# Performance work log

Measured on AMD Instinct MI355X. Metric: run time of the kernel, lower is better.

Reference implementation:

```python
import jax, jax.numpy as jnp
import numpy as np

N, E = 100000, 400000
IN_DIM, PAD_DIM, HID = 384, 3, 64

def _xavier(key, fan_in, fan_out, shape=None):
    shape = shape or (fan_in, fan_out)
    lim = float(np.sqrt(6.0 / (fan_in + fan_out)))
    return jax.random.uniform(key, shape, jnp.float32, -lim, lim)

def setup_inputs():
    key = jax.random.key(0)
    ks = jax.random.split(key, 20)
    return {
        "x": jax.random.normal(ks[0], (N, IN_DIM), jnp.float32),
        "edge_index": jax.random.randint(ks[1], (2, E), 0, N),
        "pad_state": jax.random.uniform(ks[2], (PAD_DIM,), jnp.float32, -1.0, 1.0),
        # GAT layer 1: in = IN_DIM+PAD_DIM, heads=4, out=HID per head
        "W1": _xavier(ks[3], IN_DIM + PAD_DIM, 4 * HID),
        "att_src1": _xavier(ks[4], HID, HID, (4, HID)),
        "att_dst1": _xavier(ks[5], HID, HID, (4, HID)),
        "b1": jnp.zeros((4 * HID,), jnp.float32),
        # GAT layer 2: in = 4*HID, heads=2
        "W2": _xavier(ks[6], 4 * HID, 2 * HID),
        "att_src2": _xavier(ks[7], HID, HID, (2, HID)),
        "att_dst2": _xavier(ks[8], HID, HID, (2, HID)),
        "b2": jnp.zeros((2 * HID,), jnp.float32),
        # attention-score MLP
        "aw1": _xavier(ks[9], 2 * HID, HID),
        "ab1": jnp.zeros((HID,), jnp.float32),
        "aw2": _xavier(ks[10], HID, 1),
        "ab2": jnp.zeros((1,), jnp.float32),
        # emotion gate
        "gw": _xavier(ks[11], PAD_DIM, HID),
        "gb": jnp.zeros((HID,), jnp.float32),
    }

def _gat(h_in, src, dst, W, a_src, a_dst, bias, heads):
    # PyG GATConv (eval mode): linear -> per-head LeakyReLU attention logits
    # -> edge softmax over destination -> scatter-add aggregation -> concat heads + bias
    n = h_in.shape[0]
    h = (h_in @ W).reshape(n, heads, -1)               # [N,H,C]
    al_s = jnp.einsum('nhc,hc->nh', h, a_src)          # [N,H]
    al_d = jnp.einsum('nhc,hc->nh', h, a_dst)
    e = jax.nn.leaky_relu(al_s[src] + al_d[dst], 0.2)  # [Etot,H]
    m = jax.ops.segment_max(e, dst, num_segments=n)    # stable softmax per dst
    p = jnp.exp(e - m[dst])
    denom = jax.ops.segment_sum(p, dst, num_segments=n)
    coef = p / (denom[dst] + 1e-16)
    out = jax.ops.segment_sum(h[src] * coef[:, :, None], dst, num_segments=n)
    return out.reshape(n, -1) + bias

def reference(x, edge_index, pad_state, W1, att_src1, att_dst1, b1,
              W2, att_src2, att_dst2, b2, aw1, ab1, aw2, ab2, gw, gb):
    n = x.shape[0]
    loops = jnp.arange(n, dtype=edge_index.dtype)      # add_self_loops=True default
    src = jnp.concatenate([edge_index[0], loops])
    dst = jnp.concatenate([edge_index[1], loops])
    pad_exp = jnp.broadcast_to(pad_state.reshape(1, -1), (n, pad_state.size))
    h = jnp.concatenate([x, pad_exp], axis=-1)         # [N, in_dim+pad_dim]
    h = jax.nn.elu(_gat(h, src, dst, W1, att_src1, att_dst1, b1, 4))
    h = jax.nn.elu(_gat(h, src, dst, W2, att_src2, att_dst2, b2, 2))
    gate = jax.nn.sigmoid(pad_exp @ gw + gb)           # [N,HID]
    h = h * jnp.tile(gate, (1, 2))                     # [N,2*HID]
    attn = jax.nn.sigmoid(jax.nn.relu(h @ aw1 + ab1) @ aw2 + ab2)  # [N,1]
    return h, attn
```

## Files before the change

### kernel.cpp

```cpp
#include <hip/hip_runtime.h>
#include <hip/hip_bf16.h>
#include <stdint.h>

#define IN_DIM 384
#define HID 64
#define C1 256
#define C2 128

typedef unsigned int uint32;
typedef __bf16 bf16x8 __attribute__((ext_vector_type(8)));
typedef float f32x4 __attribute__((ext_vector_type(4)));

static __device__ __forceinline__ float bf2f(unsigned short u){
    return __uint_as_float(((uint32)u) << 16);
}
static __device__ __forceinline__ unsigned short f2bf(float x){
    uint32 u = __float_as_uint(x);
    return (unsigned short)((u + 0x7FFFu + ((u >> 16) & 1u)) >> 16);
}
static __device__ __forceinline__ uint32 pack2(float a, float b){
    return (uint32)f2bf(a) | ((uint32)f2bf(b) << 16);
}

__global__ void k_zero(int* deg, int* cur, int N){
    int i = blockIdx.x*256 + threadIdx.x;
    if (i < N){ deg[i] = 0; cur[i] = 0; }
}
__global__ void k_hist(const int* __restrict__ ei, int* deg, int E){
    int i = blockIdx.x*256 + threadIdx.x;
    if (i < E) atomicAdd(&deg[ei[E + i]], 1);
}
__global__ void k_scan1(const int* __restrict__ deg, int* rowptr, int* part, int N){
    __shared__ int s[256];
    int tid = threadIdx.x;
    int i = blockIdx.x*256 + tid;
    int v = (i < N) ? deg[i] : 0;
    s[tid] = v; __syncthreads();
    for (int off = 1; off < 256; off <<= 1){
        int t = (tid >= off) ? s[tid - off] : 0;
        __syncthreads();
        s[tid] += t;
        __syncthreads();
    }
    if (i < N) rowptr[i] = s[tid] - v;
    if (tid == 255) part[blockIdx.x] = s[tid];
}
__global__ void k_scan2(int* part, int nb){
    __shared__ int s[512];
    int tid = threadIdx.x;
    int v = (tid < nb) ? part[tid] : 0;
    s[tid] = v; __syncthreads();
    for (int off = 1; off < 512; off <<= 1){
        int t = (tid >= off) ? s[tid - off] : 0;
        __syncthreads();
        s[tid] += t;
        __syncthreads();
    }
    if (tid < nb) part[tid] = s[tid] - v;
}
__global__ void k_scan3(int* rowptr, const int* __restrict__ part, int N, int E){
    int i = blockIdx.x*256 + threadIdx.x;
    if (i < N) rowptr[i] += part[blockIdx.x];
    if (i == 0) rowptr[N] = E;
}
__global__ void k_scatter(const int* __restrict__ ei, const int* __restrict__ rowptr,
                          int* cur, int* colx, int* dstx, int E){
    int i = blockIdx.x*256 + threadIdx.x;
    if (i < E){
        int d = ei[E + i];
        int pos = atomicAdd(&cur[d], 1);
        int p = rowptr[d] + pos;
        colx[p] = ei[i];
        dstx[p] = d;
    }
}

__global__ __launch_bounds__(256) void k_cvtW(const float* __restrict__ W,
        unsigned short* __restrict__ Wf, int ncol, int ntiles, int nunits){
    int unit = blockIdx.x*4 + (threadIdx.x >> 6);
    if (unit >= nunits) return;
    int l = threadIdx.x & 63;
    int s = unit / ntiles, ct = unit % ntiles;
    int col = ct*16 + (l & 15);
    int g = l >> 4;
    unsigned short o[8];
    #pragma unroll
    for (int j = 0; j < 8; j++){
        int k = s*32 + g*8 + j;
        o[j] = f2bf(W[(size_t)k*ncol + col]);
    }
    ushort4* dst = (ushort4*)&Wf[((size_t)unit*64 + l)*8];
    dst[0] = make_ushort4(o[0], o[1], o[2], o[3]);
    dst[1] = make_ushort4(o[4], o[5], o[6], o[7]);
}

__global__ __launch_bounds__(256) void k_prep(const float* __restrict__ W1,
        const float* __restrict__ pad, const float* __restrict__ gw, const float* __restrict__ gb,
        float* __restrict__ c1v, float* __restrict__ gate){
    int tid = threadIdx.x;
    c1v[tid] = pad[0]*W1[(size_t)(IN_DIM+0)*C1 + tid]
             + pad[1]*W1[(size_t)(IN_DIM+1)*C1 + tid]
             + pad[2]*W1[(size_t)(IN_DIM+2)*C1 + tid];
    if (tid < HID){
        float g = pad[0]*gw[0*HID + tid] + pad[1]*gw[1*HID + tid] + pad[2]*gw[2*HID + tid] + gb[tid];
        gate[tid] = 1.f/(1.f + __expf(-g));
    }
}

__global__ __launch_bounds__(256) void k_gemm1_mfma(const float* __restrict__ x,
        const unsigned short* __restrict__ Wf, const float* __restrict__ c1v,
        const float* __restrict__ as1, const float* __restrict__ ad1,
        unsigned short* __restrict__ h1, float* __restrict__ als, float* __restrict__ ald, int N)
{
    __shared__ unsigned short Af[2][4*64*8];
    const int tid = threadIdx.x;
    const int l   = tid & 63;
    const int w   = tid >> 6;
    const int n0  = blockIdx.x * 64;

    const int sr  = tid >> 2;
    const int kc  = tid & 3;
    const int d0  = ((sr >> 4)*64 + kc*16 + (sr & 15))*8;
    int crow = n0 + sr; if (crow > N-1) crow = N-1;
    const float* xrow = x + (size_t)crow*IN_DIM + kc*8;

    f32x4 acc[4][4];
    #pragma unroll
    for (int i = 0; i < 4; i++)
        #pragma unroll
        for (int rt = 0; rt < 4; rt++)
            acc[i][rt] = (f32x4){0.f, 0.f, 0.f, 0.f};

    float4 ra, rb;
    uint4 wcur[4], wnxt[4];

    ra = *(const float4*)(xrow + 0); rb = *(const float4*)(xrow + 4);
    {
        uint4 u;
        u.x = pack2(ra.x, ra.y); u.y = pack2(ra.z, ra.w);
        u.z = pack2(rb.x, rb.y); u.w = pack2(rb.z, rb.w);
        *(uint4*)&Af[0][d0] = u;
    }
    {
        const unsigned short* p = Wf + ((size_t)(w*4)*64 + l)*8;
        #pragma unroll
        for (int i = 0; i < 4; i++) wcur[i] = *(const uint4*)(p + (size_t)i*512);
    }
    __syncthreads();

    for (int s = 0; s < 12; ++s){
        if (s < 11){
            const float* src = xrow + (s+1)*32;
            ra = *(const float4*)(src + 0); rb = *(const float4*)(src + 4);
            const unsigned short* p = Wf + ((size_t)((s+1)*16 + w*4)*64 + l)*8;
            #pragma unroll
            for (int i = 0; i < 4; i++) wnxt[i] = *(const uint4*)(p + (size_t)i*512);
        }
        bf16x8 af[4];
        #pragma unroll
        for (int rt = 0; rt < 4; rt++)
            af[rt] = __builtin_bit_cast(bf16x8, *(const uint4*)&Af[s&1][(rt*64 + l)*8]);
        #pragma unroll
        for (int i = 0; i < 4; i++){
            bf16x8 bw = __builtin_bit_cast(bf16x8, wcur[i]);
            #pragma unroll
            for (int rt = 0; rt < 4; rt++)
                acc[i][rt] = __builtin_amdgcn_mfma_f32_16x16x32_bf16(bw, af[rt], acc[i][rt], 0, 0, 0);
        }
        if (s < 11){
            uint4 u;
            u.x = pack2(ra.x, ra.y); u.y = pack2(ra.z, ra.w);
            u.z = pack2(rb.x, rb.y); u.w = pack2(rb.z, rb.w);
            *(uint4*)&Af[(s+1)&1][d0] = u;
            __syncthreads();
            #pragma unroll
            for (int i = 0; i < 4; i++) wcur[i] = wnxt[i];
        }
    }

    const int g = l >> 4;
    float4 cvv[4], av[4], dv[4];
    #pragma unroll
    for (int i = 0; i < 4; i++){
        int cl = i*16 + g*4;
        cvv[i] = *(const float4*)&c1v[w*64 + cl];
        av[i]  = *(const float4*)&as1[w*64 + cl];
        dv[i]  = *(const float4*)&ad1[w*64 + cl];
    }
    #pragma unroll
    for (int rt = 0; rt < 4; rt++){
        int node = n0 + rt*16 + (l & 15);
        bool ok = node < N;
        float ps = 0.f, pd = 0.f;
        #pragma unroll
        for (int i = 0; i < 4; i++){
            float h0 = acc[i][rt][0] + cvv[i].x;
            float h1v = acc[i][rt][1] + cvv[i].y;
            float h2v = acc[i][rt][2] + cvv[i].z;
            float h3v = acc[i][rt][3] + cvv[i].w;
            ps += h0*av[i].x + h1v*av[i].y + h2v*av[i].z + h3v*av[i].w;
            pd += h0*dv[i].x + h1v*dv[i].y + h2v*dv[i].z + h3v*dv[i].w;
            if (ok){
                ushort4 o = make_ushort4(f2bf(h0), f2bf(h1v), f2bf(h2v), f2bf(h3v));
                *(ushort4*)&h1[(size_t)node*C1 + w*64 + i*16 + g*4] = o;
            }
        }
        ps += __shfl_xor(ps, 16, 64); ps += __shfl_xor(ps, 32, 64);
        pd += __shfl_xor(pd, 16, 64); pd += __shfl_xor(pd, 32, 64);
        if (ok && g == 0){
            als[(size_t)node*4 + w] = ps;
            ald[(size_t)node*4 + w] = pd;
        }
    }
}

__global__ __launch_bounds__(256) void k_gemm2_mfma(const unsigned short* __restrict__ x2,
        const unsigned short* __restrict__ Wf,
        const float* __restrict__ as2, const float* __restrict__ ad2,
        unsigned short* __restrict__ h2, float* __restrict__ als, float* __restrict__ ald, int N)
{
    __shared__ unsigned short Af[2][4*64*8];
    const int tid = threadIdx.x;
    const int l   = tid & 63;
    const int w   = tid >> 6;
    const int wr  = w >> 1, wc = w & 1;
    const int n0  = blockIdx.x * 64;

    const int sr  = tid >> 2;
    const int kc  = tid & 3;
    const int d0  = ((sr >> 4)*64 + kc*16 + (sr & 15))*8;
    int crow = n0 + sr; if (crow > N-1) crow = N-1;
    const unsigned short* xrow = x2 + (size_t)crow*C1 + kc*8;

    f32x4 acc[4][2];
    #pragma unroll
    for (int i = 0; i < 4; i++)
        #pragma unroll
        for (int rt = 0; rt < 2; rt++)
            acc[i][rt] = (f32x4){0.f, 0.f, 0.f, 0.f};

    uint4 p0, wcur[4], wnxt[4];
    p0 = *(const uint4*)(xrow);
    *(uint4*)&Af[0][d0] = p0;
    {
        const unsigned short* p = Wf + ((size_t)(wc*4)*64 + l)*8;
        #pragma unroll
        for (int i = 0; i < 4; i++) wcur[i] = *(const uint4*)(p + (size_t)i*512);
    }
    __syncthreads();

    for (int s = 0; s < 8; ++s){
        if (s < 7){
            p0 = *(const uint4*)(xrow + (s+1)*32);
            const unsigned short* p = Wf + ((size_t)((s+1)*8 + wc*4)*64 + l)*8;
            #pragma unroll
            for (int i = 0; i < 4; i++) wnxt[i] = *(const uint4*)(p + (size_t)i*512);
        }
        bf16x8 af[2];
        #pragma unroll
        for (int rt = 0; rt < 2; rt++)
            af[rt] = __builtin_bit_cast(bf16x8, *(const uint4*)&Af[s&1][((wr*2 + rt)*64 + l)*8]);
        #pragma unroll
        for (int i = 0; i < 4; i++){
            bf16x8 bw = __builtin_bit_cast(bf16x8, wcur[i]);
            #pragma unroll
            for (int rt = 0; rt < 2; rt++)
                acc[i][rt] = __builtin_amdgcn_mfma_f32_16x16x32_bf16(bw, af[rt], acc[i][rt], 0, 0, 0);
        }
        if (s < 7){
            *(uint4*)&Af[(s+1)&1][d0] = p0;
            __syncthreads();
            #pragma unroll
            for (int i = 0; i < 4; i++) wcur[i] = wnxt[i];
        }
    }

    const int g = l >> 4;
    float4 av[4], dv[4];
    #pragma unroll
    for (int i = 0; i < 4; i++){
        int cl = i*16 + g*4;
        av[i] = *(const float4*)&as2[wc*64 + cl];
        dv[i] = *(const float4*)&ad2[wc*64 + cl];
    }
    #pragma unroll
    for (int rt = 0; rt < 2; rt++){
        int node = n0 + wr*32 + rt*16 + (l & 15);
        bool ok = node < N;
        float ps = 0.f, pd = 0.f;
        #pragma unroll
        for (int i = 0; i < 4; i++){
            float h0 = acc[i][rt][0], h1v = acc[i][rt][1];
            float h2v = acc[i][rt][2], h3v = acc[i][rt][3];
            ps += h0*av[i].x + h1v*av[i].y + h2v*av[i].z + h3v*av[i].w;
            pd += h0*dv[i].x + h1v*dv[i].y + h2v*dv[i].z + h3v*dv[i].w;
            if (ok){
                ushort4 o = make_ushort4(f2bf(h0), f2bf(h1v), f2bf(h2v), f2bf(h3v));
                *(ushort4*)&h2[(size_t)node*C2 + wc*64 + i*16 + g*4] = o;
            }
        }
        ps += __shfl_xor(ps, 16, 64); ps += __shfl_xor(ps, 32, 64);
        pd += __shfl_xor(pd, 16, 64); pd += __shfl_xor(pd, 32, 64);
        if (ok && g == 0){
            als[(size_t)node*2 + wc] = ps;
            ald[(size_t)node*2 + wc] = pd;
        }
    }
}

template<int H>
__global__ __launch_bounds__(256) void k_elogit(const int* __restrict__ colx,
        const int* __restrict__ dstx, const float* __restrict__ als,
        const float* __restrict__ ald, float* __restrict__ ep, int E)
{
    int i = blockIdx.x*256 + threadIdx.x;
    if (i >= E) return;
    int s = colx[i], d = dstx[i];
    if constexpr (H == 4){
        float4 a = *(const float4*)&als[(size_t)s*4];
        float4 b = *(const float4*)&ald[(size_t)d*4];
        float4 e;
        e.x = a.x + b.x; e.x = fmaxf(e.x, 0.2f*e.x);
        e.y = a.y + b.y; e.y = fmaxf(e.y, 0.2f*e.y);
        e.z = a.z + b.z; e.z = fmaxf(e.z, 0.2f*e.z);
        e.w = a.w + b.w; e.w = fmaxf(e.w, 0.2f*e.w);
        *(float4*)&ep[(size_t)i*4] = e;
    } else {
        float2 a = *(const float2*)&als[(size_t)s*2];
        float2 b = *(const float2*)&ald[(size_t)d*2];
        float2 e;
        e.x = a.x + b.x; e.x = fmaxf(e.x, 0.2f*e.x);
        e.y = a.y + b.y; e.y = fmaxf(e.y, 0.2f*e.y);
        *(float2*)&ep[(size_t)i*2] = e;
    }
}

template<int H>
__global__ __launch_bounds__(256) void k_segsm(const int* __restrict__ rowptr,
        const float* __restrict__ als, const float* __restrict__ ald,
        float* __restrict__ ep, float* __restrict__ den, float* __restrict__ pSelf, int NH)
{
    int t = blockIdx.x*256 + threadIdx.x;
    if (t >= NH) return;
    int node = t / H;
    int head = t - node*H;
    int base = rowptr[node];
    int cnt  = rowptr[node+1] - base;
    float es = als[t] + ald[t];
    es = fmaxf(es, 0.2f*es);
    float m = es;
    for (int j = 0; j < cnt; j++)
        m = fmaxf(m, ep[(size_t)(base + j)*H + head]);
    float ps = __expf(es - m);
    float dn = ps;
    for (int j = 0; j < cnt; j++){
        size_t idx = (size_t)(base + j)*H + head;
        float p = __expf(ep[idx] - m);
        ep[idx] = p;
        dn += p;
    }
    den[t]   = dn;
    pSelf[t] = ps;
}

template<int H, int CPL, int LAYER>
__global__ __launch_bounds__(256) void k_gat(const unsigned short* __restrict__ hlin,
        const float* __restrict__ ep, const float* __restrict__ den, const float* __restrict__ pSelf,
        const int* __restrict__ rowptr, const int* __restrict__ colx,
        const float* __restrict__ bias, const float* __restrict__ gate,
        unsigned short* __restrict__ out_bf, float* __restrict__ out_f, int N)
{
    constexpr int C = H*64;
    constexpr uint32 RB = C*2;
    int lane = threadIdx.x & 63, wid = threadIdx.x >> 6;
    int n = blockIdx.x*4 + wid;
    if (n >= N) return;
    const int c0 = lane*CPL;
    const int head = c0 >> 6;
    const int base = rowptr[n];
    const int cnt  = rowptr[n+1] - base;
    const char* hbase = (const char*)hlin + (uint32)c0*2;

    float acc[CPL];
    {
        float psf = pSelf[(uint32)n*H + head];
        if constexpr (CPL == 4){
            ushort4 v = *(const ushort4*)(hbase + (size_t)(uint32)n*RB);
            acc[0] = psf*bf2f(v.x); acc[1] = psf*bf2f(v.y);
            acc[2] = psf*bf2f(v.z); acc[3] = psf*bf2f(v.w);
        } else {
            uint32 v = *(const uint32*)(hbase + (size_t)(uint32)n*RB);
            acc[0] = psf*bf2f((unsigned short)(v & 0xffff));
            acc[1] = psf*bf2f((unsigned short)(v >> 16));
        }
    }
    for (int i = 0; i < cnt; i += 4){
        int idx[4], sk[4];
        #pragma unroll
        for (int k = 0; k < 4; k++){
            int ii = i + k; if (ii > cnt-1) ii = cnt-1;
            idx[k] = base + ii;
        }
        #pragma unroll
        for (int k = 0; k < 4; k++) sk[k] = colx[idx[k]];
        float pk[4];
        #pragma unroll
        for (int k = 0; k < 4; k++){
            float pv = ep[(size_t)(uint32)idx[k]*H + head];
            pk[k] = (i + k < cnt) ? pv : 0.f;
        }
        if constexpr (CPL == 4){
            ushort4 h4[4];
            #pragma unroll
            for (int k = 0; k < 4; k++) h4[k] = *(const ushort4*)(hbase + (size_t)(uint32)sk[k]*RB);
            #pragma unroll
            for (int k = 0; k < 4; k++){
                acc[0] += pk[k]*bf2f(h4[k].x);
                acc[1] += pk[k]*bf2f(h4[k].y);
                acc[2] += pk[k]*bf2f(h4[k].z);
                acc[3] += pk[k]*bf2f(h4[k].w);
            }
        } else {
            uint32 h2v[4];
            #pragma unroll
            for (int k = 0; k < 4; k++) h2v[k] = *(const uint32*)(hbase + (size_t)(uint32)sk[k]*RB);
            #pragma unroll
            for (int k = 0; k < 4; k++){
                acc[0] += pk[k]*bf2f((unsigned short)(h2v[k] & 0xffff));
                acc[1] += pk[k]*bf2f((unsigned short)(h2v[k] >> 16));
            }
        }
    }

    float inv = 1.f/(den[(uint32)n*H + head] + 1e-16f);
    if constexpr (LAYER == 1){
        unsigned short o[CPL];
        #pragma unroll
        for (int j = 0; j < CPL; j++){
            float r = acc[j]*inv + bias[c0 + j];
            r = (r > 0.f) ? r : (__expf(r) - 1.f);
            o[j] = f2bf(r);
        }
        if constexpr (CPL == 4){
            ushort4 ov; ov.x = o[0]; ov.y = o[1]; ov.z = o[2]; ov.w = o[3];
            *(ushort4*)&out_bf[(size_t)n*C + c0] = ov;
        }
    } else {
        float o[CPL];
        #pragma unroll
        for (int j = 0; j < CPL; j++){
            float r = acc[j]*inv + bias[c0 + j];
            r = (r > 0.f) ? r : (__expf(r) - 1.f);
            o[j] = r*gate[(c0 + j) & 63];
        }
        if constexpr (CPL == 2){
            *(float2*)&out_f[(size_t)n*C + c0] = make_float2(o[0], o[1]);
        }
    }
}

__global__ __launch_bounds__(256) void k_attn_mfma(const float* __restrict__ outh,
        const unsigned short* __restrict__ Wfa, const float* __restrict__ ab1,
        const float* __restrict__ aw2, const float* __restrict__ ab2,
        float* __restrict__ attn, int N)
{
    __shared__ unsigned short Af[4*8*64*8];
    const int tid = threadIdx.x;
    const int l   = tid & 63;
    const int w   = tid >> 6;
    const int n0  = blockIdx.x * 128;

    const int r  = tid >> 1;
    const int kh = tid & 1;
    const int rt8 = r >> 4, rr = r & 15;
    int crow = n0 + r; if (crow > N-1) crow = N-1;
    const float* src = outh + (size_t)crow*C2 + kh*16;
    #pragma unroll
    for (int s = 0; s < 4; s++){
        float4 a = *(const float4*)(src + s*32 + 0);
        float4 b = *(const float4*)(src + s*32 + 4);
        float4 c = *(const float4*)(src + s*32 + 8);
        float4 d = *(const float4*)(src + s*32 + 12);
        uint4 u0, u1;
        u0.x = pack2(a.x, a.y); u0.y = pack2(a.z, a.w);
        u0.z = pack2(b.x, b.y); u0.w = pack2(b.z, b.w);
        u1.x = pack2(c.x, c.y); u1.y = pack2(c.z, c.w);
        u1.z = pack2(d.x, d.y); u1.w = pack2(d.z, d.w);
        int d0 = ((s*8 + rt8)*64 + (kh*2)*16 + rr)*8;
        *(uint4*)&Af[d0]       = u0;
        *(uint4*)&Af[d0 + 128] = u1;
    }
    __syncthreads();

    f32x4 acc[4][2];
    #pragma unroll
    for (int i = 0; i < 4; i++)
        #pragma unroll
        for (int rt = 0; rt < 2; rt++)
            acc[i][rt] = (f32x4){0.f, 0.f, 0.f, 0.f};

    #pragma unroll
    for (int s = 0; s < 4; s++){
        bf16x8 af[2];
        #pragma unroll
        for (int rt = 0; rt < 2; rt++)
            af[rt] = __builtin_bit_cast(bf16x8, *(const uint4*)&Af[((s*8 + w*2 + rt)*64 + l)*8]);
        #pragma unroll
        for (int i = 0; i < 4; i++){
            bf16x8 bw = __builtin_bit_cast(bf16x8, *(const uint4*)&Wfa[((size_t)(s*4 + i)*64 + l)*8]);
            #pragma unroll
            for (int rt = 0; rt < 2; rt++)
                acc[i][rt] = __builtin_amdgcn_mfma_f32_16x16x32_bf16(bw, af[rt], acc[i][rt], 0, 0, 0);
        }
    }

    const int g = l >> 4;
    float4 abv[4], awv[4];
    #pragma unroll
    for (int i = 0; i < 4; i++){
        abv[i] = *(const float4*)&ab1[i*16 + g*4];
        awv[i] = *(const float4*)&aw2[i*16 + g*4];
    }
    float b2v = ab2[0];
    #pragma unroll
    for (int rt = 0; rt < 2; rt++){
        int node = n0 + (w*2 + rt)*16 + (l & 15);
        float part = 0.f;
        #pragma unroll
        for (int i = 0; i < 4; i++){
            float v0 = fmaxf(acc[i][rt][0] + abv[i].x, 0.f);
            float v1 = fmaxf(acc[i][rt][1] + abv[i].y, 0.f);
            float v2 = fmaxf(acc[i][rt][2] + abv[i].z, 0.f);
            float v3 = fmaxf(acc[i][rt][3] + abv[i].w, 0.f);
            part += v0*awv[i].x + v1*awv[i].y + v2*awv[i].z + v3*awv[i].w;
        }
        part += __shfl_xor(part, 16, 64);
        part += __shfl_xor(part, 32, 64);
        if (g == 0 && node < N)
            attn[node] = 1.f/(1.f + __expf(-(part + b2v)));
    }
}

extern "C" void kernel_launch(void* const* d_in, const int* in_sizes, int n_in,
                              void* d_out, int out_size, void* d_ws, size_t ws_size,
                              hipStream_t stream)
{
    const float* x    = (const float*)d_in[0];
    const int*   ei   = (const int*)  d_in[1];
    const float* pad  = (const float*)d_in[2];
    const float* W1   = (const float*)d_in[3];
    const float* as1  = (const float*)d_in[4];
    const float* ad1  = (const float*)d_in[5];
    const float* b1   = (const float*)d_in[6];
    const float* W2   = (const float*)d_in[7];
    const float* as2  = (const float*)d_in[8];
    const float* ad2  = (const float*)d_in[9];
    const float* b2   = (const float*)d_in[10];
    const float* aw1  = (const float*)d_in[11];
    const float* ab1  = (const float*)d_in[12];
    const float* aw2  = (const float*)d_in[13];
    const float* ab2  = (const float*)d_in[14];
    const float* gw   = (const float*)d_in[15];
    const float* gb   = (const float*)d_in[16];

    const int N = in_sizes[0] / IN_DIM;
    const int E = in_sizes[1] / 2;

    float* outh    = (float*)d_out;
    float* outattn = outh + (size_t)N*C2;

    char* w = (char*)d_ws;
    auto alloc = [&](size_t bytes)->char*{
        char* p = w;
        w += (bytes + 255) & ~(size_t)255;
        return p;
    };
    unsigned short* h1  = (unsigned short*)alloc((size_t)N*C1*2);
    unsigned short* x2  = (unsigned short*)alloc((size_t)N*C1*2);
    unsigned short* h2  = (unsigned short*)alloc((size_t)N*C2*2);
    float* als1 = (float*)alloc((size_t)N*4*4);
    float* ald1 = (float*)alloc((size_t)N*4*4);
    float* als2 = (float*)alloc((size_t)N*2*4);
    float* ald2 = (float*)alloc((size_t)N*2*4);
    int* deg    = (int*)alloc((size_t)N*4);
    int* cur    = (int*)alloc((size_t)N*4);
    int* rowptr = (int*)alloc((size_t)(N+1)*4);
    int* colx   = (int*)alloc((size_t)E*4);
    int* dstx   = (int*)alloc((size_t)E*4);
    int* part   = (int*)alloc(512*4);
    unsigned short* Wf1 = (unsigned short*)alloc((size_t)12*16*64*8*2);
    unsigned short* Wf2 = (unsigned short*)alloc((size_t)8*8*64*8*2);
    unsigned short* Wfa = (unsigned short*)alloc((size_t)4*4*64*8*2);
    float* c1v  = (float*)alloc(C1*4);
    float* gate = (float*)alloc(HID*4);

    float* ep1    = (float*)h2;
    float* den1   = (float*)((char*)h2 + (size_t)E*16);
    float* pSelf1 = (float*)((char*)h2 + (size_t)E*16 + (size_t)N*16);
    float* ep2    = (float*)x2;
    float* den2   = (float*)((char*)x2 + (size_t)E*8);
    float* pSelf2 = (float*)((char*)x2 + (size_t)E*8 + (size_t)N*8);

    const int nbN = (N + 255)/256;
    const int nbE = (E + 255)/256;
    const int nbW = (N + 3)/4;
    const int nbG = (N + 63)/64;
    const int nbA = (N + 127)/128;

    k_cvtW <<<(192+3)/4, 256, 0, stream>>>(W1, Wf1, C1, 16, 192);
    k_cvtW <<<(64+3)/4,  256, 0, stream>>>(W2, Wf2, C2, 8, 64);
    k_cvtW <<<(16+3)/4,  256, 0, stream>>>(aw1, Wfa, HID, 4, 16);
    k_prep <<<1, 256, 0, stream>>>(W1, pad, gw, gb, c1v, gate);

    k_zero   <<<nbN, 256, 0, stream>>>(deg, cur, N);
    k_hist   <<<nbE, 256, 0, stream>>>(ei, deg, E);
    k_scan1  <<<nbN, 256, 0, stream>>>(deg, rowptr, part, N);
    k_scan2  <<<1, 512, 0, stream>>>(part, nbN);
    k_scan3  <<<nbN, 256, 0, stream>>>(rowptr, part, N, E);
    k_scatter<<<nbE, 256, 0, stream>>>(ei, rowptr, cur, colx, dstx, E);

    k_gemm1_mfma<<<nbG, 256, 0, stream>>>(x, Wf1, c1v, as1, ad1, h1, als1, ald1, N);
    k_elogit<4><<<nbE, 256, 0, stream>>>(colx, dstx, als1, ald1, ep1, E);
    k_segsm<4> <<<(N*4 + 255)/256, 256, 0, stream>>>(rowptr, als1, ald1, ep1, den1, pSelf1, N*4);
    k_gat<4,4,1><<<nbW, 256, 0, stream>>>(h1, ep1, den1, pSelf1, rowptr, colx, b1,
                                          nullptr, x2, nullptr, N);

    k_gemm2_mfma<<<nbG, 256, 0, stream>>>(x2, Wf2, as2, ad2, h2, als2, ald2, N);
    k_elogit<2><<<nbE, 256, 0, stream>>>(colx, dstx, als2, ald2, ep2, E);
    k_segsm<2> <<<(N*2 + 255)/256, 256, 0, stream>>>(rowptr, als2, ald2, ep2, den2, pSelf2, N*2);
    k_gat<2,2,2><<<nbW, 256, 0, stream>>>(h2, ep2, den2, pSelf2, rowptr, colx, b2,
                                          gate, nullptr, outh, N);

    k_attn_mfma<<<nbA, 256, 0, stream>>>(outh, Wfa, ab1, aw2, ab2, outattn, N);
}
```

Baseline: 288.6 us.

## Restructure GEMM kernels so each wave owns 16 rows and all output columns

Both GEMM kernels drop the shared-memory double-buffered A tile and the per-step block barriers. Each wave now loads its own 16 node rows directly from global memory into registers and computes every output column, reading all weight fragments from global/L2 memory. This removes LDS traffic and __syncthreads, and lets the attention-logit partials for all heads be written as one vector store per node. In exchange, weight-fragment loads per wave grow four-fold (layer 1) and the accumulator register count rises, which may lower occupancy.

Result: slower. 579.2 us (+100.7%).

```diff
diff --git a/kernel.cpp b/kernel.cpp
--- a/kernel.cpp
+++ b/kernel.cpp
@@ -112,105 +112,68 @@
         const float* __restrict__ as1, const float* __restrict__ ad1,
         unsigned short* __restrict__ h1, float* __restrict__ als, float* __restrict__ ald, int N)
 {
-    __shared__ unsigned short Af[2][4*64*8];
     const int tid = threadIdx.x;
     const int l   = tid & 63;
     const int w   = tid >> 6;
     const int n0  = blockIdx.x * 64;
 
-    const int sr  = tid >> 2;
-    const int kc  = tid & 3;
-    const int d0  = ((sr >> 4)*64 + kc*16 + (sr & 15))*8;
-    int crow = n0 + sr; if (crow > N-1) crow = N-1;
-    const float* xrow = x + (size_t)crow*IN_DIM + kc*8;
-
-    f32x4 acc[4][4];
-    #pragma unroll
-    for (int i = 0; i < 4; i++)
-        #pragma unroll
-        for (int rt = 0; rt < 4; rt++)
-            acc[i][rt] = (f32x4){0.f, 0.f, 0.f, 0.f};
-
-    float4 ra, rb;
-    uint4 wcur[4], wnxt[4];
-
-    ra = *(const float4*)(xrow + 0); rb = *(const float4*)(xrow + 4);
-    {
-        uint4 u;
-        u.x = pack2(ra.x, ra.y); u.y = pack2(ra.z, ra.w);
-        u.z = pack2(rb.x, rb.y); u.w = pack2(rb.z, rb.w);
-        *(uint4*)&Af[0][d0] = u;
-    }
-    {
-        const unsigned short* p = Wf + ((size_t)(w*4)*64 + l)*8;
-        #pragma unroll
-        for (int i = 0; i < 4; i++) wcur[i] = *(const uint4*)(p + (size_t)i*512);
-    }
-    __syncthreads();
-
-    for (int s = 0; s < 12; ++s){
-        if (s < 11){
-            const float* src = xrow + (s+1)*32;
-            ra = *(const float4*)(src + 0); rb = *(const float4*)(src + 4);
-            const unsigned short* p = Wf + ((size_t)((s+1)*16 + w*4)*64 + l)*8;
-            #pragma unroll
-            for (int i = 0; i < 4; i++) wnxt[i] = *(const uint4*)(p + (size_t)i*512);
-        }
-        bf16x8 af[4];
-        #pragma unroll
-        for (int rt = 0; rt < 4; rt++)
-            af[rt] = __builtin_bit_cast(bf16x8, *(const uint4*)&Af[s&1][(rt*64 + l)*8]);
-        #pragma unroll
-        for (int i = 0; i < 4; i++){
-            bf16x8 bw = __builtin_bit_cast(bf16x8, wcur[i]);
-            #pragma unroll
-            for (int rt = 0; rt < 4; rt++)
-                acc[i][rt] = __builtin_amdgcn_mfma_f32_16x16x32_bf16(bw, af[rt], acc[i][rt], 0, 0, 0);
-        }
-        if (s < 11){
-            uint4 u;
-            u.x = pack2(ra.x, ra.y); u.y = pack2(ra.z, ra.w);
-            u.z = pack2(rb.x, rb.y); u.w = pack2(rb.z, rb.w);
-            *(uint4*)&Af[(s+1)&1][d0] = u;
-            __syncthreads();
-            #pragma unroll
-            for (int i = 0; i < 4; i++) wcur[i] = wnxt[i];
+    const int node = n0 + w*16 + (l & 15);
+    int crow = node; if (crow > N-1) crow = N-1;
+    const float* xr = x + (size_t)crow*IN_DIM + (l >> 4)*8;
+
+    f32x4 acc[16];
+    #pragma unroll
+    for (int i = 0; i < 16; i++) acc[i] = (f32x4){0.f, 0.f, 0.f, 0.f};
+
+    float4 a0 = *(const float4*)(xr);
+    float4 a1 = *(const float4*)(xr + 4);
+
+    for (int ku = 0; ku < 12; ++ku){
+        uint4 af;
+        af.x = pack2(a0.x, a0.y); af.y = pack2(a0.z, a0.w);
+        af.z = pack2(a1.x, a1.y); af.w = pack2(a1.z, a1.w);
+        if (ku < 11){
+            a0 = *(const float4*)(xr + (ku+1)*32);
+            a1 = *(const float4*)(xr + (ku+1)*32 + 4);
+        }
+        bf16x8 afb = __builtin_bit_cast(bf16x8, af);
+        const unsigned short* wp = Wf + ((size_t)(ku*16)*64 + l)*8;
+        #pragma unroll
+        for (int i = 0; i < 16; i++){
+            bf16x8 bw = __builtin_bit_cast(bf16x8, *(const uint4*)(wp + (size_t)i*512));
+            acc[i] = __builtin_amdgcn_mfma_f32_16x16x32_bf16(bw, afb, acc[i], 0, 0, 0);
         }
     }
 
     const int g = l >> 4;
-    float4 cvv[4], av[4], dv[4];
-    #pragma unroll
-    for (int i = 0; i < 4; i++){
-        int cl = i*16 + g*4;
-        cvv[i] = *(const float4*)&c1v[w*64 + cl];
-        av[i]  = *(const float4*)&as1[w*64 + cl];
-        dv[i]  = *(const float4*)&ad1[w*64 + cl];
-    }
-    #pragma unroll
-    for (int rt = 0; rt < 4; rt++){
-        int node = n0 + rt*16 + (l & 15);
-        bool ok = node < N;
-        float ps = 0.f, pd = 0.f;
-        #pragma unroll
-        for (int i = 0; i < 4; i++){
-            float h0 = acc[i][rt][0] + cvv[i].x;
-            float h1v = acc[i][rt][1] + cvv[i].y;
-            float h2v = acc[i][rt][2] + cvv[i].z;
-            float h3v = acc[i][rt][3] + cvv[i].w;
-            ps += h0*av[i].x + h1v*av[i].y + h2v*av[i].z + h3v*av[i].w;
-            pd += h0*dv[i].x + h1v*dv[i].y + h2v*dv[i].z + h3v*dv[i].w;
-            if (ok){
-                ushort4 o = make_ushort4(f2bf(h0), f2bf(h1v), f2bf(h2v), f2bf(h3v));
-                *(ushort4*)&h1[(size_t)node*C1 + w*64 + i*16 + g*4] = o;
-            }
-        }
-        ps += __shfl_xor(ps, 16, 64); ps += __shfl_xor(ps, 32, 64);
-        pd += __shfl_xor(pd, 16, 64); pd += __shfl_xor(pd, 32, 64);
-        if (ok && g == 0){
-            als[(size_t)node*4 + w] = ps;
-            ald[(size_t)node*4 + w] = pd;
-        }
+    const bool ok = node < N;
+    float ps[4] = {0.f,0.f,0.f,0.f}, pd[4] = {0.f,0.f,0.f,0.f};
+    #pragma unroll
+    for (int i = 0; i < 16; i++){
+        int col = i*16 + g*4;
+        float4 cv = *(const float4*)&c1v[col];
+        float4 av = *(const float4*)&as1[col];
+        float4 dv = *(const float4*)&ad1[col];
+        float h0 = acc[i][0] + cv.x;
+        float h1v = acc[i][1] + cv.y;
+        float h2v = acc[i][2] + cv.z;
+        float h3v = acc[i][3] + cv.w;
+        int h = i >> 2;
+        ps[h] += h0*av.x + h1v*av.y + h2v*av.z + h3v*av.w;
+        pd[h] += h0*dv.x + h1v*dv.y + h2v*dv.z + h3v*dv.w;
+        if (ok){
+            ushort4 o = make_ushort4(f2bf(h0), f2bf(h1v), f2bf(h2v), f2bf(h3v));
+            *(ushort4*)&h1[(size_t)node*C1 + col] = o;
+        }
+    }
+    #pragma unroll
+    for (int h = 0; h < 4; h++){
+        ps[h] += __shfl_xor(ps[h], 16, 64); ps[h] += __shfl_xor(ps[h], 32, 64);
+        pd[h] += __shfl_xor(pd[h], 16, 64); pd[h] += __shfl_xor(pd[h], 32, 64);
+    }
+    if (ok && g == 0){
+        *(float4*)&als[(size_t)node*4] = make_float4(ps[0], ps[1], ps[2], ps[3]);
+        *(float4*)&ald[(size_t)node*4] = make_float4(pd[0], pd[1], pd[2], pd[3]);
     }
 }
 
@@ -219,92 +182,57 @@
         const float* __restrict__ as2, const float* __restrict__ ad2,
         unsigned short* __restrict__ h2, float* __restrict__ als, float* __restrict__ ald, int N)
 {
-    __shared__ unsigned short Af[2][4*64*8];
     const int tid = threadIdx.x;
     const int l   = tid & 63;
     const int w   = tid >> 6;
-    const int wr  = w >> 1, wc = w & 1;
     const int n0  = blockIdx.x * 64;
 
-    const int sr  = tid >> 2;
-    const int kc  = tid & 3;
-    const int d0  = ((sr >> 4)*64 + kc*16 + (sr & 15))*8;
-    int crow = n0 + sr; if (crow > N-1) crow = N-1;
-    const unsigned short* xrow = x2 + (size_t)crow*C1 + kc*8;
-
-    f32x4 acc[4][2];
-    #pragma unroll
-    for (int i = 0; i < 4; i++)
-        #pragma unroll
-        for (int rt = 0; rt < 2; rt++)
-            acc[i][rt] = (f32x4){0.f, 0.f, 0.f, 0.f};
-
-    uint4 p0, wcur[4], wnxt[4];
-    p0 = *(const uint4*)(xrow);
-    *(uint4*)&Af[0][d0] = p0;
-    {
-        const unsigned short* p = Wf + ((size_t)(wc*4)*64 + l)*8;
-        #pragma unroll
-        for (int i = 0; i < 4; i++) wcur[i] = *(const uint4*)(p + (size_t)i*512);
-    }
-    __syncthreads();
-
-    for (int s = 0; s < 8; ++s){
-        if (s < 7){
-            p0 = *(const uint4*)(xrow + (s+1)*32);
-            const unsigned short* p = Wf + ((size_t)((s+1)*8 + wc*4)*64 + l)*8;
-            #pragma unroll
-            for (int i = 0; i < 4; i++) wnxt[i] = *(const uint4*)(p + (size_t)i*512);
-        }
-        bf16x8 af[2];
-        #pragma unroll
-        for (int rt = 0; rt < 2; rt++)
-            af[rt] = __builtin_bit_cast(bf16x8, *(const uint4*)&Af[s&1][((wr*2 + rt)*64 + l)*8]);
-        #pragma unroll
-        for (int i = 0; i < 4; i++){
-            bf16x8 bw = __builtin_bit_cast(bf16x8, wcur[i]);
-            #pragma unroll
-            for (int rt = 0; rt < 2; rt++)
-                acc[i][rt] = __builtin_amdgcn_mfma_f32_16x16x32_bf16(bw, af[rt], acc[i][rt], 0, 0, 0);
-        }
-        if (s < 7){
-            *(uint4*)&Af[(s+1)&1][d0] = p0;
-            __syncthreads();
-            #pragma unroll
-            for (int i = 0; i < 4; i++) wcur[i] = wnxt[i];
+    const int node = n0 + w*16 + (l & 15);
+    int crow = node; if (crow > N-1) crow = N-1;
+    const unsigned short* xr = x2 + (size_t)crow*C1 + (l >> 4)*8;
+
+    f32x4 acc[8];
+    #pragma unroll
+    for (int i = 0; i < 8; i++) acc[i] = (f32x4){0.f, 0.f, 0.f, 0.f};
+
+    uint4 a0 = *(const uint4*)(xr);
+
+    for (int ku = 0; ku < 8; ++ku){
+        bf16x8 afb = __builtin_bit_cast(bf16x8, a0);
+        if (ku < 7) a0 = *(const uint4*)(xr + (ku+1)*32);
+        const unsigned short* wp = Wf + ((size_t)(ku*8)*64 + l)*8;
+        #pragma unroll
+        for (int i = 0; i < 8; i++){
+            bf16x8 bw = __builtin_bit_cast(bf16x8, *(const uint4*)(wp + (size_t)i*512));
+            acc[i] = __builtin_amdgcn_mfma_f32_16x16x32_bf16(bw, afb, acc[i], 0, 0, 0);
         }
     }
 
     const int g = l >> 4;
-    float4 av[4], dv[4];
-    #pragma unroll
-    for (int i = 0; i < 4; i++){
-        int cl = i*16 + g*4;
-        av[i] = *(const float4*)&as2[wc*64 + cl];
-        dv[i] = *(const float4*)&ad2[wc*64 + cl];
-    }
-    #pragma unroll
-    for (int rt = 0; rt < 2; rt++){
-        int node = n0 + wr*32 + rt*16 + (l & 15);
-        bool ok = node < N;
-        float ps = 0.f, pd = 0.f;
-        #pragma unroll
-        for (int i = 0; i < 4; i++){
-            float h0 = acc[i][rt][0], h1v = acc[i][rt][1];
-            float h2v = acc[i][rt][2], h3v = acc[i][rt][3];
-            ps += h0*av[i].x + h1v*av[i].y + h2v*av[i].z + h3v*av[i].w;
-            pd += h0*dv[i].x + h1v*dv[i].y + h2v*dv[i].z + h3v*dv[i].w;
-            if (ok){
-                ushort4 o = make_ushort4(f2bf(h0), f2bf(h1v), f2bf(h2v), f2bf(h3v));
-                *(ushort4*)&h2[(size_t)node*C2 + wc*64 + i*16 + g*4] = o;
-            }
-        }
-        ps += __shfl_xor(ps, 16, 64); ps += __shfl_xor(ps, 32, 64);
-        pd += __shfl_xor(pd, 16, 64); pd += __shfl_xor(pd, 32, 64);
-        if (ok && g == 0){
-            als[(size_t)node*2 + wc] = ps;
-            ald[(size_t)node*2 + wc] = pd;
-        }
+    const bool ok = node < N;
+    float ps[2] = {0.f,0.f}, pd[2] = {0.f,0.f};
+    #pragma unroll
+    for (int i = 0; i < 8; i++){
+        int col = i*16 + g*4;
+        float4 av = *(const float4*)&as2[col];
+        float4 dv = *(const float4*)&ad2[col];
+        float h0 = acc[i][0], h1v = acc[i][1], h2v = acc[i][2], h3v = acc[i][3];
+        int h = i >> 2;
+        ps[h] += h0*av.x + h1v*av.y + h2v*av.z + h3v*av.w;
+        pd[h] += h0*dv.x + h1v*dv.y + h2v*dv.z + h3v*dv.w;
+        if (ok){
+            ushort4 o = make_ushort4(f2bf(h0), f2bf(h1v), f2bf(h2v), f2bf(h3v));
+            *(ushort4*)&h2[(size_t)node*C2 + col] = o;
+        }
+    }
+    #pragma unroll
+    for (int h = 0; h < 2; h++){
+        ps[h] += __shfl_xor(ps[h], 16, 64); ps[h] += __shfl_xor(ps[h], 32, 64);
+        pd[h] += __shfl_xor(pd[h], 16, 64); pd[h] += __shfl_xor(pd[h], 32, 64);
+    }
+    if (ok && g == 0){
+        *(float2*)&als[(size_t)node*2] = make_float2(ps[0], ps[1]);
+        *(float2*)&ald[(size_t)node*2] = make_float2(pd[0], pd[1]);
     }
 }
 
```

## Load whole x tile into LDS upfront and drop per-step barriers in GEMM1

Applied to the files above, without the earlier changes.

The first-layer GEMM kernel now issues all 24 float4 loads of its 64-row x tile at once, converts them to bf16 and stores the full K=384 tile in shared memory (48 KB). The per-iteration double-buffered staging and its __syncthreads are removed, so the k-loop only prefetches weights. This aims to expose more memory-level parallelism on the dominant x read and to cut barrier stalls. The cost is higher register pressure and LDS use, which may lower occupancy.

Result: no change. 289.2 us (median of 2 runs) (+0.2%).

```diff
diff --git a/kernel.cpp b/kernel.cpp
--- a/kernel.cpp
+++ b/kernel.cpp
@@ -112,17 +112,30 @@
         const float* __restrict__ as1, const float* __restrict__ ad1,
         unsigned short* __restrict__ h1, float* __restrict__ als, float* __restrict__ ald, int N)
 {
-    __shared__ unsigned short Af[2][4*64*8];
+    __shared__ unsigned short Af[12*4*64*8];
     const int tid = threadIdx.x;
     const int l   = tid & 63;
     const int w   = tid >> 6;
     const int n0  = blockIdx.x * 64;
 
-    const int sr  = tid >> 2;
-    const int kc  = tid & 3;
-    const int d0  = ((sr >> 4)*64 + kc*16 + (sr & 15))*8;
-    int crow = n0 + sr; if (crow > N-1) crow = N-1;
-    const float* xrow = x + (size_t)crow*IN_DIM + kc*8;
+    const int srow = w*16 + (l & 15);
+    const int kc   = l >> 4;
+    int crow = n0 + srow; if (crow > N-1) crow = N-1;
+    const float* xr = x + (size_t)crow*IN_DIM + kc*8;
+
+    float4 a0[12], a1[12];
+    #pragma unroll
+    for (int j = 0; j < 12; j++){
+        a0[j] = *(const float4*)(xr + j*32);
+        a1[j] = *(const float4*)(xr + j*32 + 4);
+    }
+    #pragma unroll
+    for (int j = 0; j < 12; j++){
+        uint4 u;
+        u.x = pack2(a0[j].x, a0[j].y); u.y = pack2(a0[j].z, a0[j].w);
+        u.z = pack2(a1[j].x, a1[j].y); u.w = pack2(a1[j].z, a1[j].w);
+        *(uint4*)&Af[((j*4 + w)*64 + l)*8] = u;
+    }
 
     f32x4 acc[4][4];
     #pragma unroll
@@ -131,16 +144,7 @@
         for (int rt = 0; rt < 4; rt++)
             acc[i][rt] = (f32x4){0.f, 0.f, 0.f, 0.f};
 
-    float4 ra, rb;
     uint4 wcur[4], wnxt[4];
-
-    ra = *(const float4*)(xrow + 0); rb = *(const float4*)(xrow + 4);
-    {
-        uint4 u;
-        u.x = pack2(ra.x, ra.y); u.y = pack2(ra.z, ra.w);
-        u.z = pack2(rb.x, rb.y); u.w = pack2(rb.z, rb.w);
-        *(uint4*)&Af[0][d0] = u;
-    }
     {
         const unsigned short* p = Wf + ((size_t)(w*4)*64 + l)*8;
         #pragma unroll
@@ -148,18 +152,16 @@
     }
     __syncthreads();
 
-    for (int s = 0; s < 12; ++s){
-        if (s < 11){
-            const float* src = xrow + (s+1)*32;
-            ra = *(const float4*)(src + 0); rb = *(const float4*)(src + 4);
-            const unsigned short* p = Wf + ((size_t)((s+1)*16 + w*4)*64 + l)*8;
+    for (int ku = 0; ku < 12; ++ku){
+        if (ku < 11){
+            const unsigned short* p = Wf + ((size_t)((ku+1)*16 + w*4)*64 + l)*8;
             #pragma unroll
             for (int i = 0; i < 4; i++) wnxt[i] = *(const uint4*)(p + (size_t)i*512);
         }
         bf16x8 af[4];
         #pragma unroll
         for (int rt = 0; rt < 4; rt++)
-            af[rt] = __builtin_bit_cast(bf16x8, *(const uint4*)&Af[s&1][(rt*64 + l)*8]);
+            af[rt] = __builtin_bit_cast(bf16x8, *(const uint4*)&Af[((ku*4 + rt)*64 + l)*8]);
         #pragma unroll
         for (int i = 0; i < 4; i++){
             bf16x8 bw = __builtin_bit_cast(bf16x8, wcur[i]);
@@ -167,12 +169,7 @@
             for (int rt = 0; rt < 4; rt++)
                 acc[i][rt] = __builtin_amdgcn_mfma_f32_16x16x32_bf16(bw, af[rt], acc[i][rt], 0, 0, 0);
         }
-        if (s < 11){
-            uint4 u;
-            u.x = pack2(ra.x, ra.y); u.y = pack2(ra.z, ra.w);
-            u.z = pack2(rb.x, rb.y); u.w = pack2(rb.z, rb.w);
-            *(uint4*)&Af[(s+1)&1][d0] = u;
-            __syncthreads();
+        if (ku < 11){
             #pragma unroll
             for (int i = 0; i < 4; i++) wcur[i] = wnxt[i];
         }
```
